# Performance work log

Measured on AMD Instinct MI355X. Metric: run time of the kernel, lower is better.

The kernel has to match this reference:

```python
import jax, jax.numpy as jnp
import numpy as np

NZ, NC = 100, 2
FEAT_NUMBER, FEATURE_DIM = 8192, 1024
B = 8192
BN_EPS = 1e-5
GUMBEL_EPS = 0.001
TEMP = 0.1


def _batchnorm(h, gamma, beta):
    # torch BatchNorm1d training mode: biased batch statistics
    mu = jnp.mean(h, axis=0, keepdims=True)
    var = jnp.var(h, axis=0, keepdims=True)
    return (h - mu) * jax.lax.rsqrt(var + BN_EPS) * gamma + beta


def setup_inputs() -> dict:
    key = jax.random.key(0)
    ks = jax.random.split(key, 16)
    def glorot(k, shape):
        lim = 1.0 / np.sqrt(shape[0])
        return jax.random.uniform(k, shape, jnp.float32, -lim, lim)
    return {
        "x": jax.random.normal(ks[0], (B, NZ), jnp.float32),
        "y": jax.random.uniform(ks[1], (B, NC), jnp.float32),
        "W1": glorot(ks[2], (NZ + NC, 256)), "b1": jnp.zeros((256,), jnp.float32),
        "g1": jnp.ones((256,), jnp.float32), "be1": jnp.zeros((256,), jnp.float32),
        "W2": glorot(ks[3], (256, 64)), "b2": jnp.zeros((64,), jnp.float32),
        "g2": jnp.ones((64,), jnp.float32), "be2": jnp.zeros((64,), jnp.float32),
        "W3": glorot(ks[4], (64, FEAT_NUMBER)), "b3": jnp.zeros((FEAT_NUMBER,), jnp.float32),
        "codebook": jax.random.normal(ks[5], (FEAT_NUMBER, FEATURE_DIM), jnp.float32),
    }


def reference(x, y, W1, b1, g1, be1, W2, b2, g2, be2, W3, b3, codebook):
    z = jnp.concatenate([x, y], axis=-1)                       # [B, nz+nc]
    h = jax.nn.relu(_batchnorm(z @ W1 + b1, g1, be1))          # [B, 256]
    h = jax.nn.relu(_batchnorm(h @ W2 + b2, g2, be2))          # [B, 64]
    logits = h @ W3 + b3                                       # [B, feat_number]

    # gumbel noise: U = eps*rand; g = -log(-log(U+eps)+eps)
    U = GUMBEL_EPS * jax.random.uniform(jax.random.key(42), logits.shape, jnp.float32)
    g = -jnp.log(-jnp.log(U + GUMBEL_EPS) + GUMBEL_EPS)
    y_soft = jax.nn.softmax((logits + g) / TEMP, axis=-1)

    # straight-through one-hot
    ind = jnp.argmax(y_soft, axis=-1)
    y_hard = jax.nn.one_hot(ind, FEAT_NUMBER, dtype=y_soft.dtype)
    z_st = jax.lax.stop_gradient(y_hard - y_soft) + y_soft     # [B, feat_number]

    # weighted codebook sum == matmul (avoids [B,F,D] broadcast intermediate)
    return jnp.einsum('bf,fd->bd', z_st, codebook)             # [B, feature_dim]
```

## Files before the change

kernel.cpp:

```cpp
#include <hip/hip_runtime.h>
#include <math.h>

#define B_ROWS   8192
#define NZ       100
#define NC       2
#define H1       256
#define H2       64
#define FEATN    8192
#define FDIM     1024
#define RROWS    16
#define NTILE    (FEATN / 16)
#define A1ROWS   16
#define A1BLKS   (B_ROWS / A1ROWS)
#define CONVBLKS 256
#define A2BLKS   (B_ROWS / 4)

typedef __attribute__((ext_vector_type(8))) short short8;
typedef __attribute__((ext_vector_type(4))) float f32x4;

__device__ __forceinline__ unsigned rotl32(unsigned v, int r) {
    return (v << r) | (v >> (32 - r));
}
__device__ __forceinline__ unsigned threefry_bits(unsigned lo) {
    const unsigned ks0 = 0u, ks1 = 42u, ks2 = 0x1BD11BDAu ^ 42u;
    unsigned x0 = 0u + ks0;
    unsigned x1 = lo + ks1;
#define TF_R4(a,b,c,d) \
    x0 += x1; x1 = rotl32(x1,a); x1 ^= x0; \
    x0 += x1; x1 = rotl32(x1,b); x1 ^= x0; \
    x0 += x1; x1 = rotl32(x1,c); x1 ^= x0; \
    x0 += x1; x1 = rotl32(x1,d); x1 ^= x0;
    TF_R4(13,15,26,6);  x0 += ks1; x1 += ks2 + 1u;
    TF_R4(17,29,16,24); x0 += ks2; x1 += ks0 + 2u;
    TF_R4(13,15,26,6);  x0 += ks0; x1 += ks1 + 3u;
    TF_R4(17,29,16,24); x0 += ks1; x1 += ks2 + 4u;
    TF_R4(13,15,26,6);  x0 += ks2; x1 += ks0 + 5u;
#undef TF_R4
    return x0 ^ x1;
}
__device__ __forceinline__ float gumbel_g(unsigned flat) {
    unsigned bits = threefry_bits(flat);
    float u  = __uint_as_float((bits >> 9) | 0x3f800000u) - 1.0f;
    float U  = 0.001f * u;
    float t1 = U + 0.001f;
    float L1 = (float)log((double)t1);
    float A  = 0.001f - L1;
    float L2 = (float)log((double)A);
    return -L2;
}

__device__ __forceinline__ unsigned short f2bf(float x) {
    unsigned u = __float_as_uint(x);
    u += 0x7fffu + ((u >> 16) & 1u);
    return (unsigned short)(u >> 16);
}
__device__ __forceinline__ unsigned fmono(float x) {
    unsigned b = __float_as_uint(x);
    return (b & 0x80000000u) ? ~b : (b | 0x80000000u);
}

__device__ __forceinline__ float dppmax16(float v) {
    int y;
    y = __builtin_amdgcn_update_dpp(0, __float_as_int(v), 0xB1,  0xF, 0xF, true);
    v = fmaxf(v, __int_as_float(y));
    y = __builtin_amdgcn_update_dpp(0, __float_as_int(v), 0x4E,  0xF, 0xF, true);
    v = fmaxf(v, __int_as_float(y));
    y = __builtin_amdgcn_update_dpp(0, __float_as_int(v), 0x141, 0xF, 0xF, true);
    v = fmaxf(v, __int_as_float(y));
    y = __builtin_amdgcn_update_dpp(0, __float_as_int(v), 0x140, 0xF, 0xF, true);
    v = fmaxf(v, __int_as_float(y));
    return v;
}

__global__ __launch_bounds__(256) void k_a1(
    const float* __restrict__ x, const float* __restrict__ y,
    const float* __restrict__ W1, const float* __restrict__ b1,
    const float* __restrict__ W3,
    float* __restrict__ a1, double* __restrict__ p1, double* __restrict__ p2,
    unsigned short* __restrict__ w3s, float* __restrict__ maxw)
{
    const int t = threadIdx.x;

    if (blockIdx.x >= A1BLKS) {
        const int job  = (blockIdx.x - A1BLKS) * 256 + t;
        const int T    = job >> 7;
        const int rem  = job & 127;
        const int kh   = rem >> 6;
        const int l    = rem & 63;
        const int quad = l >> 4, col = l & 15;
        const float* src = W3 + (size_t)(kh * 32 + quad * 8) * FEATN + T * 16 + col;
        unsigned short v[8];
        float mx = 0.0f;
#pragma unroll
        for (int jj = 0; jj < 8; ++jj) {
            float xv = src[(size_t)jj * FEATN];
            mx = fmaxf(mx, fabsf(xv));
            v[jj] = f2bf(xv);
        }
        uint4 o;
        o.x = (unsigned)v[0] | ((unsigned)v[1] << 16);
        o.y = (unsigned)v[2] | ((unsigned)v[3] << 16);
        o.z = (unsigned)v[4] | ((unsigned)v[5] << 16);
        o.w = (unsigned)v[6] | ((unsigned)v[7] << 16);
        ((uint4*)w3s)[job] = o;
#pragma unroll
        for (int off = 32; off; off >>= 1) mx = fmaxf(mx, __shfl_xor(mx, off));
        __shared__ float wred[4];
        if ((t & 63) == 0) wred[t >> 6] = mx;
        __syncthreads();
        if (t == 0) {
            float m = fmaxf(fmaxf(wred[0], wred[1]), fmaxf(wred[2], wred[3]));
            atomicMax((unsigned*)maxw, __float_as_uint(m));
        }
        return;
    }

    const int j  = t;
    const int b0 = blockIdx.x * A1ROWS;

    __shared__ float xs[A1ROWS * NZ];
    __shared__ float ys[A1ROWS * NC];
    for (int q = t; q < A1ROWS * NZ; q += 256) xs[q] = x[(size_t)b0 * NZ + q];
    if (t < A1ROWS * NC) ys[t] = y[b0 * NC + t];
    __syncthreads();

    double acc[A1ROWS];
#pragma unroll
    for (int r = 0; r < A1ROWS; ++r) acc[r] = 0.0;
    for (int i = 0; i < NZ; ++i) {
        float w = W1[i * H1 + j];
#pragma unroll
        for (int r = 0; r < A1ROWS; ++r)
            acc[r] += (double)xs[r * NZ + i] * (double)w;
    }
#pragma unroll
    for (int i = 0; i < NC; ++i) {
        float w = W1[(NZ + i) * H1 + j];
#pragma unroll
        for (int r = 0; r < A1ROWS; ++r)
            acc[r] += (double)ys[r * NC + i] * (double)w;
    }
    double bb = (double)b1[j];
    double s = 0.0, s2 = 0.0;
#pragma unroll
    for (int r = 0; r < A1ROWS; ++r) {
        float v = (float)(acc[r] + bb);
        a1[(b0 + r) * H1 + j] = v;
        double dv = (double)v;
        s += dv; s2 += dv * dv;
    }
    p1[blockIdx.x * H1 + j] = s;
    p2[blockIdx.x * H1 + j] = s2;
}

__global__ __launch_bounds__(256) void k_stats2(
    const double* __restrict__ p1, const double* __restrict__ p2,
    int nprt, int ncol,
    const float* __restrict__ gamma, const float* __restrict__ beta,
    float* __restrict__ scale, float* __restrict__ shift)
{
    const int j = blockIdx.x, t = threadIdx.x;
    double s = 0.0, s2 = 0.0;
    for (int g = t; g < nprt; g += 256) {
        s  += p1[(size_t)g * ncol + j];
        s2 += p2[(size_t)g * ncol + j];
    }
#pragma unroll
    for (int off = 32; off; off >>= 1) {
        s  += __shfl_xor(s, off);
        s2 += __shfl_xor(s2, off);
    }
    __shared__ double ws1[4], ws2[4];
    if ((t & 63) == 0) { ws1[t >> 6] = s; ws2[t >> 6] = s2; }
    __syncthreads();
    if (t == 0) {
        s  = (ws1[0] + ws1[1]) + (ws1[2] + ws1[3]);
        s2 = (ws2[0] + ws2[1]) + (ws2[2] + ws2[3]);
        double mean = s * (1.0 / B_ROWS);
        double var  = s2 * (1.0 / B_ROWS) - mean * mean;
        double rstd = 1.0 / sqrt(var + 1e-5);
        double sc   = (double)gamma[j] * rstd;
        scale[j] = (float)sc;
        shift[j] = (float)((double)beta[j] - mean * sc);
    }
}

__global__ __launch_bounds__(256) void k_a2(
    const float* __restrict__ a1,
    const float* __restrict__ sc1, const float* __restrict__ sh1,
    const float* __restrict__ W2, const float* __restrict__ b2,
    float* __restrict__ a2, double* __restrict__ p1, double* __restrict__ p2)
{
    const int t  = threadIdx.x;
    const int k  = t & 63;
    const int rr = t >> 6;
    const int b  = blockIdx.x * 4 + rr;
    double acc = 0.0;
    for (int j = 0; j < H1; ++j) {
        float h = fmaxf(fmaf(a1[b * H1 + j], sc1[j], sh1[j]), 0.0f);
        acc += (double)h * (double)W2[j * H2 + k];
    }
    float v = (float)(acc + (double)b2[k]);
    a2[b * H2 + k] = v;

    __shared__ double ls[256], ls2[256];
    ls[t]  = (double)v;
    ls2[t] = (double)v * (double)v;
    __syncthreads();
    if (t < 64) {
        double s  = (ls[t]  + ls[t + 64])  + (ls[t + 128]  + ls[t + 192]);
        double s2 = (ls2[t] + ls2[t + 64]) + (ls2[t + 128] + ls2[t + 192]);
        p1[blockIdx.x * H2 + t] = s;
        p2[blockIdx.x * H2 + t] = s2;
    }
}

__global__ __launch_bounds__(512)
__attribute__((amdgpu_waves_per_eu(4, 4)))
void k_main(
    const float* __restrict__ a2,
    const float* __restrict__ sc2, const float* __restrict__ sh2,
    const float* __restrict__ W3, const float* __restrict__ b3,
    const unsigned short* __restrict__ w3s, const float* __restrict__ maxw,
    const float* __restrict__ codebook, float* __restrict__ out)
{
    const int t    = threadIdx.x;
    const int wv   = t >> 6;
    const int lane = t & 63;
    const int quad = lane >> 4, col = lane & 15;
    const int b0   = blockIdx.x * RROWS;

    __shared__ __align__(16) float h2T[64][17];
    __shared__ float fineT[NTILE][17];
    __shared__ float thrS[RROWS];
    __shared__ unsigned long long best[RROWS];
    __shared__ unsigned short wl[RROWS * NTILE];
    __shared__ int wlN;
    __shared__ int rowInd[RROWS];
    __shared__ float maxwS;

    if (t == 0) { maxwS = maxw[0]; wlN = 0; }
    for (int q = t; q < RROWS * 64; q += 512) {
        int j = q >> 4, r = q & 15;
        float v = a2[(b0 + r) * H2 + j];
        h2T[j][r] = fmaxf(fmaf(v, sc2[j], sh2[j]), 0.0f);
    }
    __syncthreads();

    short8 aF0, aF1;
#pragma unroll
    for (int jj = 0; jj < 8; ++jj) {
        aF0[jj] = (short)f2bf(h2T[quad * 8 + jj][col]);
        aF1[jj] = (short)f2bf(h2T[32 + quad * 8 + jj][col]);
    }

    {
        const uint4* wp  = (const uint4*)w3s + (size_t)wv * 8192 + lane;
        const float* b3p = b3 + wv * 1024 + col;
        for (int s = 0; s < 8; ++s) {
            uint4 c[8], d[8];
            float bb[8];
#pragma unroll
            for (int u = 0; u < 8; ++u) {
                c[u]  = wp[u * 128];
                d[u]  = wp[u * 128 + 64];
                bb[u] = b3p[u * 16];
            }
#pragma unroll
            for (int u = 0; u < 8; ++u) {
                f32x4 acc = {bb[u], bb[u], bb[u], bb[u]};
                acc = __builtin_amdgcn_mfma_f32_16x16x32_bf16(
                          aF0, *(const short8*)&c[u], acc, 0, 0, 0);
                acc = __builtin_amdgcn_mfma_f32_16x16x32_bf16(
                          aF1, *(const short8*)&d[u], acc, 0, 0, 0);
                float m0 = dppmax16(acc[0]);
                float m1 = dppmax16(acc[1]);
                float m2 = dppmax16(acc[2]);
                float m3 = dppmax16(acc[3]);
                if (col == 0) {
                    const int T = (wv * 8 + s) * 8 + u;
                    fineT[T][quad * 4 + 0] = m0;
                    fineT[T][quad * 4 + 1] = m1;
                    fineT[T][quad * 4 + 2] = m2;
                    fineT[T][quad * 4 + 3] = m3;
                }
            }
            wp += 1024; b3p += 128;
        }
    }
    __syncthreads();

    {
        const int r = t >> 5, cc = t & 31;
        float s = fabsf(h2T[2 * cc][r]) + fabsf(h2T[2 * cc + 1][r]);
        float gmv = -1e30f;
#pragma unroll
        for (int k = 0; k < 16; ++k) gmv = fmaxf(gmv, fineT[cc + 32 * k][r]);
#pragma unroll
        for (int off = 1; off < 32; off <<= 1) {
            s   += __shfl_xor(s, off);
            gmv  = fmaxf(gmv, __shfl_xor(gmv, off));
        }
        if (cc == 0) {
            float e = s * maxwS * (1.0f / 256.0f);
            thrS[r] = gmv - (0.1068f + e + 1e-3f);
            best[r] = 0ull;
        }
    }
    __syncthreads();

    {
        const int r = t >> 5, cc = t & 31;
        const float th = thrS[r];
#pragma unroll
        for (int k = 0; k < 16; ++k) {
            const int T = cc + 32 * k;
            if (fineT[T][r] >= th) {
                int idx = atomicAdd(&wlN, 1);
                wl[idx] = (unsigned short)((r << 9) | T);
            }
        }
    }
    __syncthreads();

    {
        const int n = wlN;
        const int g = lane >> 4;
        for (int i = wv * 4; i < n; i += 32) {
            const int  ci  = i + g;
            const bool act = (ci < n);
            const int  e   = act ? wl[ci] : 0;
            const int  r   = e >> 9;
            const int  T   = e & 511;
            const int  f   = T * 16 + col;
            float acc = b3[f];
            const float* wcol = W3 + f;
#pragma unroll 8
            for (int j = 0; j < 64; ++j) {
                acc = fmaf(h2T[j][r], *wcol, acc);
                wcol += FEATN;
            }
            if (act && acc >= thrS[r]) {
                float sc = acc + gumbel_g((unsigned)(b0 + r) * (unsigned)FEATN + (unsigned)f);
                unsigned long long pk = ((unsigned long long)fmono(sc) << 32)
                                      | (unsigned)(FEATN - 1 - f);
                atomicMax(&best[r], pk);
            }
        }
    }
    __syncthreads();
    if (t < RROWS) {
        rowInd[t] = (FEATN - 1 - (int)(best[t] & 0xFFFFFFFFull)) & (FEATN - 1);
    }
    __syncthreads();

    {
        const int rr = t >> 8, tt = t & 255;
        for (int rp = 0; rp < RROWS / 2; ++rp) {
            const int r = rp * 2 + rr;
            const int ind = rowInd[r];
            const float4* src = (const float4*)(codebook + (size_t)ind * FDIM);
            float4*       dst = (float4*)(out + (size_t)(b0 + r) * FDIM);
            dst[tt] = src[tt];
        }
    }
}

extern "C" void kernel_launch(void* const* d_in, const int* in_sizes, int n_in,
                              void* d_out, int out_size, void* d_ws, size_t ws_size,
                              hipStream_t stream)
{
    const float* x   = (const float*)d_in[0];
    const float* y   = (const float*)d_in[1];
    const float* W1  = (const float*)d_in[2];
    const float* b1  = (const float*)d_in[3];
    const float* g1  = (const float*)d_in[4];
    const float* be1 = (const float*)d_in[5];
    const float* W2  = (const float*)d_in[6];
    const float* b2  = (const float*)d_in[7];
    const float* g2  = (const float*)d_in[8];
    const float* be2 = (const float*)d_in[9];
    const float* W3  = (const float*)d_in[10];
    const float* b3  = (const float*)d_in[11];
    const float* cb  = (const float*)d_in[12];
    float* out = (float*)d_out;

    float* ws  = (float*)d_ws;
    float* a1  = ws;
    float* a2  = a1 + B_ROWS * H1;
    float* sc1 = a2 + B_ROWS * H2;
    float* sh1 = sc1 + H1;
    float* sc2 = sh1 + H1;
    float* sh2 = sc2 + H2;
    double* p1 = (double*)(sh2 + H2);
    double* p2 = p1 + A2BLKS * H2;
    unsigned short* w3s = (unsigned short*)(p2 + A2BLKS * H2);
    float* maxw = (float*)(w3s + NTILE * 2 * 64 * 8);

    hipMemsetAsync(maxw, 0, 4, stream);
    k_a1    <<<A1BLKS + CONVBLKS, 256, 0, stream>>>(x, y, W1, b1, W3,
                                                    a1, p1, p2, w3s, maxw);
    k_stats2<<<H1, 256, 0, stream>>>(p1, p2, A1BLKS, H1, g1, be1, sc1, sh1);
    k_a2    <<<A2BLKS, 256, 0, stream>>>(a1, sc1, sh1, W2, b2, a2, p1, p2);
    k_stats2<<<H2, 256, 0, stream>>>(p1, p2, A2BLKS, H2, g2, be2, sc2, sh2);
    k_main  <<<B_ROWS / RROWS, 512, 0, stream>>>(a2, sc2, sh2, W3, b3,
                                                 w3s, maxw, cb, out);
}
```

Before: 238.5 us.

## Transpose LDS activations, tile k_a2 over 16 rows, swap MFMA operands for row max

```diff
diff --git a/kernel.cpp b/kernel.cpp
--- a/kernel.cpp
+++ b/kernel.cpp
@@ -13,7 +13,8 @@
 #define A1ROWS   16
 #define A1BLKS   (B_ROWS / A1ROWS)
 #define CONVBLKS 256
-#define A2BLKS   (B_ROWS / 4)
+#define A2ROWS   16
+#define A2BLKS   (B_ROWS / A2ROWS)
 
 typedef __attribute__((ext_vector_type(8))) short short8;
 typedef __attribute__((ext_vector_type(4))) float f32x4;
@@ -59,19 +60,6 @@
     return (b & 0x80000000u) ? ~b : (b | 0x80000000u);
 }
 
-__device__ __forceinline__ float dppmax16(float v) {
-    int y;
-    y = __builtin_amdgcn_update_dpp(0, __float_as_int(v), 0xB1,  0xF, 0xF, true);
-    v = fmaxf(v, __int_as_float(y));
-    y = __builtin_amdgcn_update_dpp(0, __float_as_int(v), 0x4E,  0xF, 0xF, true);
-    v = fmaxf(v, __int_as_float(y));
-    y = __builtin_amdgcn_update_dpp(0, __float_as_int(v), 0x141, 0xF, 0xF, true);
-    v = fmaxf(v, __int_as_float(y));
-    y = __builtin_amdgcn_update_dpp(0, __float_as_int(v), 0x140, 0xF, 0xF, true);
-    v = fmaxf(v, __int_as_float(y));
-    return v;
-}
-
 __global__ __launch_bounds__(256) void k_a1(
     const float* __restrict__ x, const float* __restrict__ y,
     const float* __restrict__ W1, const float* __restrict__ b1,
@@ -118,27 +106,51 @@
     const int j  = t;
     const int b0 = blockIdx.x * A1ROWS;
 
-    __shared__ float xs[A1ROWS * NZ];
-    __shared__ float ys[A1ROWS * NC];
-    for (int q = t; q < A1ROWS * NZ; q += 256) xs[q] = x[(size_t)b0 * NZ + q];
-    if (t < A1ROWS * NC) ys[t] = y[b0 * NC + t];
+    __shared__ __align__(16) float xs[NZ][16];
+    __shared__ __align__(16) float ys[NC][16];
+    for (int q = t; q < A1ROWS * NZ; q += 256) {
+        int r = q / NZ, i = q - r * NZ;
+        xs[i][r] = x[(size_t)b0 * NZ + q];
+    }
+    if (t < A1ROWS * NC) {
+        int r = t >> 1, i = t & 1;
+        ys[i][r] = y[b0 * NC + t];
+    }
     __syncthreads();
 
     double acc[A1ROWS];
 #pragma unroll
     for (int r = 0; r < A1ROWS; ++r) acc[r] = 0.0;
     for (int i = 0; i < NZ; ++i) {
-        float w = W1[i * H1 + j];
-#pragma unroll
-        for (int r = 0; r < A1ROWS; ++r)
-            acc[r] += (double)xs[r * NZ + i] * (double)w;
+        double wd = (double)W1[i * H1 + j];
+        const float4 x0 = *(const float4*)&xs[i][0];
+        const float4 x1 = *(const float4*)&xs[i][4];
+        const float4 x2 = *(const float4*)&xs[i][8];
+        const float4 x3 = *(const float4*)&xs[i][12];
+        acc[0]  += (double)x0.x * wd; acc[1]  += (double)x0.y * wd;
+        acc[2]  += (double)x0.z * wd; acc[3]  += (double)x0.w * wd;
+        acc[4]  += (double)x1.x * wd; acc[5]  += (double)x1.y * wd;
+        acc[6]  += (double)x1.z * wd; acc[7]  += (double)x1.w * wd;
+        acc[8]  += (double)x2.x * wd; acc[9]  += (double)x2.y * wd;
+        acc[10] += (double)x2.z * wd; acc[11] += (double)x2.w * wd;
+        acc[12] += (double)x3.x * wd; acc[13] += (double)x3.y * wd;
+        acc[14] += (double)x3.z * wd; acc[15] += (double)x3.w * wd;
     }
 #pragma unroll
     for (int i = 0; i < NC; ++i) {
-        float w = W1[(NZ + i) * H1 + j];
-#pragma unroll
-        for (int r = 0; r < A1ROWS; ++r)
-            acc[r] += (double)ys[r * NC + i] * (double)w;
+        double wd = (double)W1[(NZ + i) * H1 + j];
+        const float4 y0 = *(const float4*)&ys[i][0];
+        const float4 y1 = *(const float4*)&ys[i][4];
+        const float4 y2 = *(const float4*)&ys[i][8];
+        const float4 y3 = *(const float4*)&ys[i][12];
+        acc[0]  += (double)y0.x * wd; acc[1]  += (double)y0.y * wd;
+        acc[2]  += (double)y0.z * wd; acc[3]  += (double)y0.w * wd;
+        acc[4]  += (double)y1.x * wd; acc[5]  += (double)y1.y * wd;
+        acc[6]  += (double)y1.z * wd; acc[7]  += (double)y1.w * wd;
+        acc[8]  += (double)y2.x * wd; acc[9]  += (double)y2.y * wd;
+        acc[10] += (double)y2.z * wd; acc[11] += (double)y2.w * wd;
+        acc[12] += (double)y3.x * wd; acc[13] += (double)y3.y * wd;
+        acc[14] += (double)y3.z * wd; acc[15] += (double)y3.w * wd;
     }
     double bb = (double)b1[j];
     double s = 0.0, s2 = 0.0;
@@ -193,25 +205,52 @@
 {
     const int t  = threadIdx.x;
     const int k  = t & 63;
-    const int rr = t >> 6;
-    const int b  = blockIdx.x * 4 + rr;
-    double acc = 0.0;
+    const int rg = t >> 6;
+    const int b0 = blockIdx.x * A2ROWS;
+
+    __shared__ __align__(16) float hs[H1][20];
+    __shared__ double ps[4][64], ps2[4][64];
+
+    {
+        const float sct = sc1[t], sht = sh1[t];
+#pragma unroll 4
+        for (int rr = 0; rr < A2ROWS; ++rr) {
+            float v = a1[(size_t)(b0 + rr) * H1 + t];
+            hs[t][rr] = fmaxf(fmaf(v, sct, sht), 0.0f);
+        }
+    }
+    __syncthreads();
+
+    const int r0 = rg * 4;
+    double acc0 = 0.0, acc1 = 0.0, acc2 = 0.0, acc3 = 0.0;
     for (int j = 0; j < H1; ++j) {
-        float h = fmaxf(fmaf(a1[b * H1 + j], sc1[j], sh1[j]), 0.0f);
-        acc += (double)h * (double)W2[j * H2 + k];
-    }
-    float v = (float)(acc + (double)b2[k]);
-    a2[b * H2 + k] = v;
-
-    __shared__ double ls[256], ls2[256];
-    ls[t]  = (double)v;
-    ls2[t] = (double)v * (double)v;
+        double wd = (double)W2[j * H2 + k];
+        const float4 h4 = *(const float4*)&hs[j][r0];
+        acc0 += (double)h4.x * wd;
+        acc1 += (double)h4.y * wd;
+        acc2 += (double)h4.z * wd;
+        acc3 += (double)h4.w * wd;
+    }
+    const double bb = (double)b2[k];
+    float v0 = (float)(acc0 + bb);
+    float v1 = (float)(acc1 + bb);
+    float v2 = (float)(acc2 + bb);
+    float v3 = (float)(acc3 + bb);
+    a2[(b0 + r0 + 0) * H2 + k] = v0;
+    a2[(b0 + r0 + 1) * H2 + k] = v1;
+    a2[(b0 + r0 + 2) * H2 + k] = v2;
+    a2[(b0 + r0 + 3) * H2 + k] = v3;
+
+    double s  = (double)v0 + (double)v1 + (double)v2 + (double)v3;
+    double s2 = (double)v0 * (double)v0 + (double)v1 * (double)v1
+              + (double)v2 * (double)v2 + (double)v3 * (double)v3;
+    ps[rg][k] = s; ps2[rg][k] = s2;
     __syncthreads();
     if (t < 64) {
-        double s  = (ls[t]  + ls[t + 64])  + (ls[t + 128]  + ls[t + 192]);
-        double s2 = (ls2[t] + ls2[t + 64]) + (ls2[t + 128] + ls2[t + 192]);
-        p1[blockIdx.x * H2 + t] = s;
-        p2[blockIdx.x * H2 + t] = s2;
+        double S  = (ps[0][t]  + ps[1][t])  + (ps[2][t]  + ps[3][t]);
+        double S2 = (ps2[0][t] + ps2[1][t]) + (ps2[2][t] + ps2[3][t]);
+        p1[blockIdx.x * H2 + t] = S;
+        p2[blockIdx.x * H2 + t] = S2;
     }
 }
 
@@ -255,37 +294,30 @@
     }
 
     {
-        const uint4* wp  = (const uint4*)w3s + (size_t)wv * 8192 + lane;
-        const float* b3p = b3 + wv * 1024 + col;
+        const uint4*  wp = (const uint4*)w3s + (size_t)wv * 8192 + lane;
+        const float4* bq = (const float4*)b3 + wv * 256 + quad;
         for (int s = 0; s < 8; ++s) {
             uint4 c[8], d[8];
-            float bb[8];
+            float4 bb[8];
 #pragma unroll
             for (int u = 0; u < 8; ++u) {
                 c[u]  = wp[u * 128];
                 d[u]  = wp[u * 128 + 64];
-                bb[u] = b3p[u * 16];
+                bb[u] = bq[u * 4];
             }
 #pragma unroll
             for (int u = 0; u < 8; ++u) {
-                f32x4 acc = {bb[u], bb[u], bb[u], bb[u]};
+                f32x4 acc = {bb[u].x, bb[u].y, bb[u].z, bb[u].w};
                 acc = __builtin_amdgcn_mfma_f32_16x16x32_bf16(
-                          aF0, *(const short8*)&c[u], acc, 0, 0, 0);
+                          *(const short8*)&c[u], aF0, acc, 0, 0, 0);
                 acc = __builtin_amdgcn_mfma_f32_16x16x32_bf16(
-                          aF1, *(const short8*)&d[u], acc, 0, 0, 0);
-                float m0 = dppmax16(acc[0]);
-                float m1 = dppmax16(acc[1]);
-                float m2 = dppmax16(acc[2]);
-                float m3 = dppmax16(acc[3]);
-                if (col == 0) {
-                    const int T = (wv * 8 + s) * 8 + u;
-                    fineT[T][quad * 4 + 0] = m0;
-                    fineT[T][quad * 4 + 1] = m1;
-                    fineT[T][quad * 4 + 2] = m2;
-                    fineT[T][quad * 4 + 3] = m3;
-                }
+                          *(const short8*)&d[u], aF1, acc, 0, 0, 0);
+                float m = fmaxf(fmaxf(acc[0], acc[1]), fmaxf(acc[2], acc[3]));
+                m = fmaxf(m, __shfl_xor(m, 16));
+                m = fmaxf(m, __shfl_xor(m, 32));
+                if (lane < 16) fineT[(wv * 8 + s) * 8 + u][lane] = m;
             }
-            wp += 1024; b3p += 128;
+            wp += 1024; bq += 32;
         }
     }
     __syncthreads();
@@ -393,8 +425,8 @@
     float* sc2 = sh1 + H1;
     float* sh2 = sc2 + H2;
     double* p1 = (double*)(sh2 + H2);
-    double* p2 = p1 + A2BLKS * H2;
-    unsigned short* w3s = (unsigned short*)(p2 + A2BLKS * H2);
+    double* p2 = p1 + A1BLKS * H1;
+    unsigned short* w3s = (unsigned short*)(p2 + A1BLKS * H1);
     float* maxw = (float*)(w3s + NTILE * 2 * 64 * 8);
 
     hipMemsetAsync(maxw, 0, 4, stream);
```

Result: faster. 214.5 us (-10.1%).
